# Kernel tuning notes

Hardware: AMD Instinct MI355X
Metric: run time of the kernel (lower is better)

The kernel has to match this reference:

```python
import jax, jax.numpy as jnp
import numpy as np

TEMPERATURE = 0.07
BASE_TEMPERATURE = 0.07
L_MAX = 16  # max number of session labels per dialogue
NEG_INF = -1e30


def setup_inputs() -> dict:
    key = jax.random.key(0)
    k1, k2, k3 = jax.random.split(key, 3)
    B, T, H = 128, 1024, 256
    features = jax.random.normal(k1, (B, T, H), dtype=jnp.float32)
    dialogue_lengths = jax.random.randint(k2, (B,), 1, T + 1)
    labels = jax.random.randint(k3, (B, T), 0, L_MAX)
    return {"features": features, "dialogue_lengths": dialogue_lengths, "labels": labels}


def reference(features, dialogue_lengths, labels):
    B, T, H = features.shape
    valid = jnp.arange(T)[None, :] < dialogue_lengths[:, None]            # [B,T]
    # one-hot label assignment, zeroed at padded positions
    oh = (labels[..., None] == jnp.arange(L_MAX)[None, None, :]) & valid[..., None]
    ohf = oh.astype(features.dtype)                                       # [B,T,L]
    counts = ohf.sum(axis=1)                                              # [B,L]
    # per-dialogue, per-label prototype = mean of member features
    proto_sum = jnp.einsum('btl,bth->blh', ohf, features)                 # [B,L,H]
    prototypes = proto_sum / jnp.maximum(counts, 1.0)[..., None]          # [B,L,H]
    # anchor-vs-prototype logits
    logits = jnp.einsum('bth,blh->btl', features, prototypes) / TEMPERATURE
    present = counts > 0                                                  # [B,L]
    logits = jnp.where(present[:, None, :], logits, NEG_INF)
    log_prob = jax.nn.log_softmax(logits, axis=-1)                        # [B,T,L]
    # mask is one-hot on each token's own label -> mean_log_prob_pos is log_prob at own label
    pos = jnp.take_along_axis(log_prob, labels[..., None], axis=-1)[..., 0]  # [B,T]
    tok_loss = -(TEMPERATURE / BASE_TEMPERATURE) * pos
    per_dialogue = jnp.sum(jnp.where(valid, tok_loss, 0.0), axis=1) / dialogue_lengths.astype(features.dtype)
    return per_dialogue.mean()
```

## Files before the change

### kernel.cpp

```cpp
#include <hip/hip_runtime.h>
#include <math.h>

#define B 128
#define T 1024
#define H 256
#define L 16
#define INV_TEMP (1.0f/0.07f)
#define NEG_INF -1e30f


__global__ __launch_bounds__(256) void proto_kernel(
    const float* __restrict__ feat, const int* __restrict__ dlen,
    const int* __restrict__ labels, float* __restrict__ ws_proto,
    int* __restrict__ ws_cnt) {
  __shared__ float acc[4][L * 128];
  __shared__ int labs[256];
  __shared__ int cnt[L];

  const int bx = blockIdx.x;
  const int b = bx >> 3;
  const int chunk = (bx >> 2) & 1;
  const int seg = bx & 3;
  const int tid = threadIdx.x;
  const int w = tid >> 6;
  const int lane = tid & 63;

  for (int i = tid; i < 4 * L * 128; i += 256) ((float*)acc)[i] = 0.f;
  labs[tid] = labels[(size_t)b * T + seg * 256 + tid];
  if (chunk == 0 && tid < L) cnt[tid] = 0;
  __syncthreads();

  const int len = dlen[b];

  if (chunk == 0 && (seg * 256 + tid) < len) atomicAdd(&cnt[labs[tid]], 1);

  int nt = len - seg * 256 - w * 64;
  if (nt > 64) nt = 64;
  const float2* fbase = (const float2*)(feat +
      ((size_t)b * T + seg * 256 + w * 64) * H + chunk * 128);
  float* a = acc[w];

  for (int j = 0; j < nt; ++j) {
    float2 f = fbase[(size_t)j * (H / 2) + lane];
    const int lab = labs[w * 64 + j];
    float2* p = (float2*)&a[lab * 128 + lane * 2];
    float2 v = *p;
    v.x += f.x; v.y += f.y;
    *p = v;
  }
  __syncthreads();

  float* gp = ws_proto + (size_t)b * L * H + chunk * 128;
  for (int e = tid; e < L * 128; e += 256) {
    const float s = acc[0][e] + acc[1][e] + acc[2][e] + acc[3][e];
    const int l = e >> 7, c = e & 127;
    atomicAdd(&gp[l * H + c], s);
  }
  if (chunk == 0 && tid < L) atomicAdd(&ws_cnt[b * L + tid], cnt[tid]);
}

__global__ __launch_bounds__(256) void dots_kernel(
    const float* __restrict__ feat, const int* __restrict__ dlen,
    const float* __restrict__ ws_proto, const int* __restrict__ ws_cnt,
    float* __restrict__ ws_dots) {
  __shared__ float pr[L * 128];
  __shared__ int cnts[L];

  const int bx = blockIdx.x;
  const int b = bx >> 2;
  const int seg2 = (bx >> 1) & 1;
  const int half = bx & 1;
  const int tid = threadIdx.x;

  if (tid < L) cnts[tid] = ws_cnt[b * L + tid];
  __syncthreads();

  const float* gp = ws_proto + (size_t)b * L * H + half * 128;
  for (int i = tid; i < L * 128; i += 256) {
    const int l = i >> 7, c = i & 127;
    const int cn = cnts[l];
    pr[i] = gp[l * H + c] * (cn > 0 ? 1.f / (float)cn : 0.f);
  }
  __syncthreads();

  const int tA = seg2 * 512 + tid;
  const float4* fA = (const float4*)(feat + ((size_t)b * T + tA) * H + half * 128);
  const float4* fB = (const float4*)((const float*)fA + 256 * H);

  float dot[2][L];
#pragma unroll
  for (int l = 0; l < L; ++l) { dot[0][l] = 0.f; dot[1][l] = 0.f; }

  for (int c8 = 0; c8 < 4; ++c8) {
    float4 fa[8], fb[8];
#pragma unroll
    for (int j = 0; j < 8; ++j) {
      fa[j] = fA[c8 * 8 + j];
      fb[j] = fB[c8 * 8 + j];
    }
#pragma unroll
    for (int j = 0; j < 8; ++j) {
#pragma unroll
      for (int l = 0; l < L; ++l) {
        const float4 p = *(const float4*)&pr[l * 128 + c8 * 32 + j * 4];
        dot[0][l] += fa[j].x * p.x + fa[j].y * p.y + fa[j].z * p.z + fa[j].w * p.w;
        dot[1][l] += fb[j].x * p.x + fb[j].y * p.y + fb[j].z * p.z + fb[j].w * p.w;
      }
    }
  }

  float* dA = ws_dots + ((size_t)half * B * T + (size_t)b * T + tA) * L;
  float* dB = dA + 256 * L;
#pragma unroll
  for (int q = 0; q < 4; ++q) {
    ((float4*)dA)[q] = make_float4(dot[0][q*4], dot[0][q*4+1], dot[0][q*4+2], dot[0][q*4+3]);
    ((float4*)dB)[q] = make_float4(dot[1][q*4], dot[1][q*4+1], dot[1][q*4+2], dot[1][q*4+3]);
  }
}

__global__ __launch_bounds__(256) void loss_kernel(
    const int* __restrict__ dlen, const int* __restrict__ labels,
    const int* __restrict__ ws_cnt, const float* __restrict__ ws_dots,
    float* __restrict__ out) {
  __shared__ int cnts[L];
  __shared__ float red[256];

  const int b = blockIdx.x >> 2;
  const int seg = blockIdx.x & 3;
  const int tid = threadIdx.x;

  if (tid < L) cnts[tid] = ws_cnt[b * L + tid];
  __syncthreads();

  const int len = dlen[b];
  const int t = seg * 256 + tid;
  float tok = 0.f;

  if (t < len) {
    const float* d0 = ws_dots + ((size_t)b * T + t) * L;
    const float* d1 = d0 + (size_t)B * T * L;
    float lg[L];
#pragma unroll
    for (int l = 0; l < L; ++l) {
      const float d = d0[l] + d1[l];
      lg[l] = (cnts[l] > 0) ? d * INV_TEMP : NEG_INF;
    }
    float m = lg[0];
#pragma unroll
    for (int l = 1; l < L; ++l) m = fmaxf(m, lg[l]);
    float se = 0.f;
#pragma unroll
    for (int l = 0; l < L; ++l) se += expf(lg[l] - m);
    const float lsp = m + logf(se);

    const int lab = labels[(size_t)b * T + t];
    float pos = 0.f;
#pragma unroll
    for (int l = 0; l < L; ++l) pos += (l == lab) ? lg[l] : 0.f;

    tok = lsp - pos;
  }

  red[tid] = tok;
  __syncthreads();
#pragma unroll
  for (int s = 128; s > 0; s >>= 1) {
    if (tid < s) red[tid] += red[tid + s];
    __syncthreads();
  }
  if (tid == 0) atomicAdd(out, red[0] / ((float)len * (float)B));
}

extern "C" void kernel_launch(void* const* d_in, const int* in_sizes, int n_in,
                              void* d_out, int out_size, void* d_ws, size_t ws_size,
                              hipStream_t stream) {
  const float* feat = (const float*)d_in[0];
  const int* dlen = (const int*)d_in[1];
  const int* labels = (const int*)d_in[2];
  float* out = (float*)d_out;

  float* ws_proto = (float*)d_ws;
  int* ws_cnt = (int*)(ws_proto + (size_t)B * L * H);
  float* ws_dots = (float*)(ws_cnt + (size_t)B * L);

  hipMemsetAsync(d_ws, 0, ((size_t)B * L * H + B * L) * sizeof(float), stream);
  hipMemsetAsync(out, 0, sizeof(float), stream);

  proto_kernel<<<B * 8, 256, 0, stream>>>(feat, dlen, labels, ws_proto, ws_cnt);
  dots_kernel<<<B * 4, 256, 0, stream>>>(feat, dlen, ws_proto, ws_cnt, ws_dots);
  loss_kernel<<<B * 4, 256, 0, stream>>>(dlen, labels, ws_cnt, ws_dots, out);
}
```

Baseline: 252.1 us.

## Replace global atomics with per-segment partial prototypes and widen dots tiling

Each proto block now writes its partial prototype sums and counts into a per-segment slot instead of doing atomicAdd, and the dots and loss kernels reduce the four slots when loading. This removes the workspace memset and the global atomics. Segments entirely past the dialogue length skip the feature reads and just write zeros, and the per-token accumulation loop is unrolled by four. The dots kernel processes four token groups per thread with half as many blocks, which reuses each LDS prototype read across more tokens but raises register pressure and lowers parallelism.

```diff
diff --git a/kernel.cpp b/kernel.cpp
--- a/kernel.cpp
+++ b/kernel.cpp
@@ -11,8 +11,8 @@
 
 __global__ __launch_bounds__(256) void proto_kernel(
     const float* __restrict__ feat, const int* __restrict__ dlen,
-    const int* __restrict__ labels, float* __restrict__ ws_proto,
-    int* __restrict__ ws_cnt) {
+    const int* __restrict__ labels, float* __restrict__ ws_pp,
+    int* __restrict__ ws_cntp) {
   __shared__ float acc[4][L * 128];
   __shared__ int labs[256];
   __shared__ int cnt[L];
@@ -25,12 +25,19 @@
   const int w = tid >> 6;
   const int lane = tid & 63;
 
+  const int len = dlen[b];
+  float* op = ws_pp + (((size_t)b * 4 + seg) * L) * H + chunk * 128;
+
+  if (seg * 256 >= len) {
+    for (int e = tid; e < L * 128; e += 256) op[(e >> 7) * H + (e & 127)] = 0.f;
+    if (chunk == 0 && tid < L) ws_cntp[(b * 4 + seg) * L + tid] = 0;
+    return;
+  }
+
   for (int i = tid; i < 4 * L * 128; i += 256) ((float*)acc)[i] = 0.f;
   labs[tid] = labels[(size_t)b * T + seg * 256 + tid];
-  if (chunk == 0 && tid < L) cnt[tid] = 0;
-  __syncthreads();
-
-  const int len = dlen[b];
+  if (tid < L) cnt[tid] = 0;
+  __syncthreads();
 
   if (chunk == 0 && (seg * 256 + tid) < len) atomicAdd(&cnt[labs[tid]], 1);
 
@@ -40,87 +47,114 @@
       ((size_t)b * T + seg * 256 + w * 64) * H + chunk * 128);
   float* a = acc[w];
 
-  for (int j = 0; j < nt; ++j) {
+  int j = 0;
+  for (; j + 4 <= nt; j += 4) {
+    float2 f0 = fbase[(size_t)(j + 0) * (H / 2) + lane];
+    float2 f1 = fbase[(size_t)(j + 1) * (H / 2) + lane];
+    float2 f2 = fbase[(size_t)(j + 2) * (H / 2) + lane];
+    float2 f3 = fbase[(size_t)(j + 3) * (H / 2) + lane];
+    const int l0 = labs[w * 64 + j + 0];
+    const int l1 = labs[w * 64 + j + 1];
+    const int l2 = labs[w * 64 + j + 2];
+    const int l3 = labs[w * 64 + j + 3];
+    float2* p0 = (float2*)&a[l0 * 128 + lane * 2];
+    { float2 v = *p0; v.x += f0.x; v.y += f0.y; *p0 = v; }
+    float2* p1 = (float2*)&a[l1 * 128 + lane * 2];
+    { float2 v = *p1; v.x += f1.x; v.y += f1.y; *p1 = v; }
+    float2* p2 = (float2*)&a[l2 * 128 + lane * 2];
+    { float2 v = *p2; v.x += f2.x; v.y += f2.y; *p2 = v; }
+    float2* p3 = (float2*)&a[l3 * 128 + lane * 2];
+    { float2 v = *p3; v.x += f3.x; v.y += f3.y; *p3 = v; }
+  }
+  for (; j < nt; ++j) {
     float2 f = fbase[(size_t)j * (H / 2) + lane];
     const int lab = labs[w * 64 + j];
     float2* p = (float2*)&a[lab * 128 + lane * 2];
-    float2 v = *p;
-    v.x += f.x; v.y += f.y;
-    *p = v;
-  }
-  __syncthreads();
-
-  float* gp = ws_proto + (size_t)b * L * H + chunk * 128;
+    float2 v = *p; v.x += f.x; v.y += f.y; *p = v;
+  }
+  __syncthreads();
+
   for (int e = tid; e < L * 128; e += 256) {
     const float s = acc[0][e] + acc[1][e] + acc[2][e] + acc[3][e];
-    const int l = e >> 7, c = e & 127;
-    atomicAdd(&gp[l * H + c], s);
-  }
-  if (chunk == 0 && tid < L) atomicAdd(&ws_cnt[b * L + tid], cnt[tid]);
+    op[(e >> 7) * H + (e & 127)] = s;
+  }
+  if (chunk == 0 && tid < L) ws_cntp[(b * 4 + seg) * L + tid] = cnt[tid];
 }
 
 __global__ __launch_bounds__(256) void dots_kernel(
-    const float* __restrict__ feat, const int* __restrict__ dlen,
-    const float* __restrict__ ws_proto, const int* __restrict__ ws_cnt,
-    float* __restrict__ ws_dots) {
+    const float* __restrict__ feat, const float* __restrict__ ws_pp,
+    const int* __restrict__ ws_cntp, float* __restrict__ ws_dots) {
   __shared__ float pr[L * 128];
   __shared__ int cnts[L];
 
   const int bx = blockIdx.x;
-  const int b = bx >> 2;
-  const int seg2 = (bx >> 1) & 1;
+  const int b = bx >> 1;
   const int half = bx & 1;
   const int tid = threadIdx.x;
 
-  if (tid < L) cnts[tid] = ws_cnt[b * L + tid];
-  __syncthreads();
-
-  const float* gp = ws_proto + (size_t)b * L * H + half * 128;
+  if (tid < L) {
+    const int* cp = ws_cntp + b * 4 * L + tid;
+    cnts[tid] = cp[0] + cp[L] + cp[2 * L] + cp[3 * L];
+  }
+  __syncthreads();
+
+  const float* gp = ws_pp + ((size_t)b * 4 * L) * H + half * 128;
   for (int i = tid; i < L * 128; i += 256) {
     const int l = i >> 7, c = i & 127;
+    const float s = gp[l * H + c] + gp[(L + l) * H + c] +
+                    gp[(2 * L + l) * H + c] + gp[(3 * L + l) * H + c];
     const int cn = cnts[l];
-    pr[i] = gp[l * H + c] * (cn > 0 ? 1.f / (float)cn : 0.f);
-  }
-  __syncthreads();
-
-  const int tA = seg2 * 512 + tid;
-  const float4* fA = (const float4*)(feat + ((size_t)b * T + tA) * H + half * 128);
-  const float4* fB = (const float4*)((const float*)fA + 256 * H);
-
-  float dot[2][L];
-#pragma unroll
-  for (int l = 0; l < L; ++l) { dot[0][l] = 0.f; dot[1][l] = 0.f; }
-
-  for (int c8 = 0; c8 < 4; ++c8) {
-    float4 fa[8], fb[8];
-#pragma unroll
-    for (int j = 0; j < 8; ++j) {
-      fa[j] = fA[c8 * 8 + j];
-      fb[j] = fB[c8 * 8 + j];
-    }
-#pragma unroll
-    for (int j = 0; j < 8; ++j) {
+    pr[i] = s * (cn > 0 ? 1.f / (float)cn : 0.f);
+  }
+  __syncthreads();
+
+  const float4* fv[4];
+#pragma unroll
+  for (int k = 0; k < 4; ++k) {
+    const int t = k * 256 + tid;
+    fv[k] = (const float4*)(feat + ((size_t)b * T + t) * H + half * 128);
+  }
+
+  float dot[4][L];
+#pragma unroll
+  for (int k = 0; k < 4; ++k)
+#pragma unroll
+    for (int l = 0; l < L; ++l) dot[k][l] = 0.f;
+
+  for (int cb = 0; cb < 8; ++cb) {
+    float4 f[4][4];
+#pragma unroll
+    for (int k = 0; k < 4; ++k)
+#pragma unroll
+      for (int q = 0; q < 4; ++q) f[k][q] = fv[k][cb * 4 + q];
+#pragma unroll
+    for (int q = 0; q < 4; ++q) {
 #pragma unroll
       for (int l = 0; l < L; ++l) {
-        const float4 p = *(const float4*)&pr[l * 128 + c8 * 32 + j * 4];
-        dot[0][l] += fa[j].x * p.x + fa[j].y * p.y + fa[j].z * p.z + fa[j].w * p.w;
-        dot[1][l] += fb[j].x * p.x + fb[j].y * p.y + fb[j].z * p.z + fb[j].w * p.w;
+        const float4 p = *(const float4*)&pr[l * 128 + cb * 16 + q * 4];
+#pragma unroll
+        for (int k = 0; k < 4; ++k) {
+          dot[k][l] += f[k][q].x * p.x + f[k][q].y * p.y +
+                       f[k][q].z * p.z + f[k][q].w * p.w;
+        }
       }
     }
   }
 
-  float* dA = ws_dots + ((size_t)half * B * T + (size_t)b * T + tA) * L;
-  float* dB = dA + 256 * L;
-#pragma unroll
-  for (int q = 0; q < 4; ++q) {
-    ((float4*)dA)[q] = make_float4(dot[0][q*4], dot[0][q*4+1], dot[0][q*4+2], dot[0][q*4+3]);
-    ((float4*)dB)[q] = make_float4(dot[1][q*4], dot[1][q*4+1], dot[1][q*4+2], dot[1][q*4+3]);
+#pragma unroll
+  for (int k = 0; k < 4; ++k) {
+    const int t = k * 256 + tid;
+    float4* d = (float4*)(ws_dots + (((size_t)half * B + b) * T + t) * L);
+#pragma unroll
+    for (int q = 0; q < 4; ++q)
+      d[q] = make_float4(dot[k][q * 4], dot[k][q * 4 + 1],
+                         dot[k][q * 4 + 2], dot[k][q * 4 + 3]);
   }
 }
 
 __global__ __launch_bounds__(256) void loss_kernel(
     const int* __restrict__ dlen, const int* __restrict__ labels,
-    const int* __restrict__ ws_cnt, const float* __restrict__ ws_dots,
+    const int* __restrict__ ws_cntp, const float* __restrict__ ws_dots,
     float* __restrict__ out) {
   __shared__ int cnts[L];
   __shared__ float red[256];
@@ -129,7 +163,10 @@
   const int seg = blockIdx.x & 3;
   const int tid = threadIdx.x;
 
-  if (tid < L) cnts[tid] = ws_cnt[b * L + tid];
+  if (tid < L) {
+    const int* cp = ws_cntp + b * 4 * L + tid;
+    cnts[tid] = cp[0] + cp[L] + cp[2 * L] + cp[3 * L];
+  }
   __syncthreads();
 
   const int len = dlen[b];
@@ -179,14 +216,12 @@
   const int* labels = (const int*)d_in[2];
   float* out = (float*)d_out;
 
-  float* ws_proto = (float*)d_ws;
-  int* ws_cnt = (int*)(ws_proto + (size_t)B * L * H);
-  float* ws_dots = (float*)(ws_cnt + (size_t)B * L);
-
-  hipMemsetAsync(d_ws, 0, ((size_t)B * L * H + B * L) * sizeof(float), stream);
+  float* ws_pp = (float*)d_ws;
+  int* ws_cntp = (int*)(ws_pp + (size_t)B * 4 * L * H);
+  float* ws_dots = (float*)(ws_cntp + (size_t)B * 4 * L);
+
   hipMemsetAsync(out, 0, sizeof(float), stream);
-
-  proto_kernel<<<B * 8, 256, 0, stream>>>(feat, dlen, labels, ws_proto, ws_cnt);
-  dots_kernel<<<B * 4, 256, 0, stream>>>(feat, dlen, ws_proto, ws_cnt, ws_dots);
-  loss_kernel<<<B * 4, 256, 0, stream>>>(dlen, labels, ws_cnt, ws_dots, out);
-}
+  proto_kernel<<<B * 8, 256, 0, stream>>>(feat, dlen, labels, ws_pp, ws_cntp);
+  dots_kernel<<<B * 2, 256, 0, stream>>>(feat, ws_pp, ws_cntp, ws_dots);
+  loss_kernel<<<B * 4, 256, 0, stream>>>(dlen, labels, ws_cntp, ws_dots, out);
+}
```

New measurement: 234.4 us. 7.0% less time.
